# Kernel optimization log

Measured on AMD Instinct MI355X. Metric: run time of the kernel, lower is better.

Reference implementation:

```python
import jax, jax.numpy as jnp
import numpy as np

B_PAIR = 4      # anchor/positive pairs; total batch = 2*B_PAIR
NUM = 4096      # keypoints per cloud
C_FEAT = 640    # descriptor dim
NB_ITER = 5


def _rigid_transform(a, b, weights):
    # a: (B,M,3), b: (B,M,3), weights: (B,M) -> (B,3,4)
    wn = weights[..., None] / (jnp.sum(weights[..., None], axis=1, keepdims=True) + 1e-5)
    centroid_a = jnp.sum(a * wn, axis=1)            # (B,3)
    centroid_b = jnp.sum(b * wn, axis=1)
    a_c = a - centroid_a[:, None, :]
    b_c = b - centroid_b[:, None, :]
    cov = jnp.swapaxes(a_c, -2, -1) @ (b_c * wn)    # (B,3,3)
    u, s, vh = jnp.linalg.svd(cov, full_matrices=False)
    v = jnp.swapaxes(vh, -2, -1)                    # torch.svd returns v, jax returns vh
    rot_pos = v @ jnp.swapaxes(u, -2, -1)
    v_neg = v.at[:, :, 2].multiply(-1.0)
    rot_neg = v_neg @ jnp.swapaxes(u, -2, -1)
    rot = jnp.where(jnp.linalg.det(rot_pos)[:, None, None] > 0, rot_pos, rot_neg)
    trans = -rot @ centroid_a[:, :, None] + centroid_b[:, :, None]
    return jnp.concatenate((rot, trans), axis=2)    # (B,3,4)


def _uot_forward(point_features, point_coords, gamma, epsilon):
    feats = point_features[..., 0]                  # (2B, C, N)
    twoB, _, N = feats.shape
    B = twoB // 2
    feat1 = jnp.transpose(feats[:B], (0, 2, 1))     # (B, N, C)
    feat2 = jnp.transpose(feats[B:], (0, 2, 1))
    coords = point_coords.reshape(twoB, -1, 4)
    coords1 = coords[:B, :, 1:]                     # (B, N, 3)
    coords2 = coords[B:, :, 1:]

    eps = jnp.exp(epsilon) + 0.03                   # scalar (1,)
    gam = jnp.exp(gamma)

    f1 = feat1 / jnp.sqrt(jnp.sum(feat1**2, -1, keepdims=True) + 1e-8)
    f2 = feat2 / jnp.sqrt(jnp.sum(feat2**2, -1, keepdims=True) + 1e-8)
    Cmat = 1.0 - jnp.einsum('bnc,bmc->bnm', f1, f2)  # (B,N,N) cosine cost
    K = jnp.exp(-Cmat / eps)

    power = gam / (gam + eps)
    inv_n = jnp.asarray(1.0 / N, K.dtype)
    a = jnp.full((B, N, 1), inv_n, K.dtype)
    prob1 = jnp.full((B, N, 1), inv_n, K.dtype)
    prob2 = jnp.full((B, N, 1), inv_n, K.dtype)
    b = prob2
    for _ in range(NB_ITER):                        # unrolled unbalanced Sinkhorn
        KTa = jnp.matmul(jnp.swapaxes(K, 1, 2), a)  # (B,N,1)
        b = jnp.power(prob2 / (KTa + 1e-8), power)
        Kb = jnp.matmul(K, b)
        a = jnp.power(prob1 / (Kb + 1e-8), power)
    T = a * K * jnp.swapaxes(b, 1, 2)               # (B,N,N) transport plan

    row_sum = jnp.sum(T, axis=-1, keepdims=True)    # (B,N,1)
    sinkhorn_matches = jnp.matmul(T, coords2) / (row_sum + 1e-8)  # (B,N,3)
    transform = _rigid_transform(coords1, sinkhorn_matches, row_sum[..., 0])
    return T, sinkhorn_matches, transform


def setup_inputs() -> dict:
    key = jax.random.key(0)
    k1, k2 = jax.random.split(key)
    point_features = jax.random.normal(k1, (2 * B_PAIR, C_FEAT, NUM, 1), dtype=jnp.float32)
    point_coords = jax.random.normal(k2, (2 * B_PAIR * NUM, 4), dtype=jnp.float32) * 10.0
    gamma = jnp.zeros((1,), jnp.float32)
    epsilon = jnp.zeros((1,), jnp.float32)
    return {"point_features": point_features, "point_coords": point_coords,
            "gamma": gamma, "epsilon": epsilon}


def reference(point_features, point_coords, gamma, epsilon):
    return _uot_forward(point_features, point_coords, gamma, epsilon)
```

## Files before the change

kernel.cpp:

```cpp
#include <hip/hip_runtime.h>
#include <hip/hip_bf16.h>
#include <math.h>

#define NB 4
#define N 4096
#define CF 640

typedef _Float16 f16;
typedef _Float16 f16x8 __attribute__((ext_vector_type(8)));
typedef _Float16 f16x4 __attribute__((ext_vector_type(4)));
typedef float    f32x4 __attribute__((ext_vector_type(4)));
typedef unsigned int u32;
typedef unsigned short u16;

#define OFF_FNT    0ll
#define OFF_RNORM  (OFF_FNT   + 8ll*N*CF*2)
#define OFF_AVEC   (OFF_RNORM + 8ll*N*4)
#define OFF_BVEC   (OFF_AVEC  + (long long)NB*N*4)
#define OFF_KTAP   (OFF_BVEC  + (long long)NB*N*4)
#define OFF_KH     (OFF_KTAP  + (long long)NB*16*N*4)
#define WS_REQ_H   (OFF_KH    + (long long)NB*N*N*2)

__device__ inline void async_copy16(void* lds, const void* g) {
    __builtin_amdgcn_global_load_lds(
        (const __attribute__((address_space(1))) u32*)g,
        (__attribute__((address_space(3))) u32*)lds,
        16, 0, 0);
}

__global__ __launch_bounds__(256) void rnorm_kernel(const float* __restrict__ pf,
                                                    float* __restrict__ rnorm) {
    int idx = blockIdx.x * 256 + threadIdx.x;
    int n = idx & (N - 1);
    int b = idx >> 12;
    const float* src = pf + (size_t)b * CF * N + n;
    float s = 0.f;
    for (int c = 0; c < CF; ++c) { float v = src[(size_t)c * N]; s = fmaf(v, v, s); }
    rnorm[idx] = 1.0f / sqrtf(s + 1e-8f);
}

__global__ __launch_bounds__(256) void transpose_kernel(const float* __restrict__ pf,
                                                        const float* __restrict__ rnorm,
                                                        f16* __restrict__ fnT) {
    __shared__ float tile[64][65];
    int b  = blockIdx.z;
    int c0 = blockIdx.x * 64;
    int n1 = blockIdx.y * 64;
    int t  = threadIdx.x;

    int c_l = t >> 4;
    int n_l4 = (t & 15) * 4;
    #pragma unroll
    for (int i = 0; i < 4; ++i) {
        int c = c_l + i * 16;
        float4 v = *(const float4*)(pf + (size_t)(b * CF + c0 + c) * N + n1 + n_l4);
        tile[c][n_l4 + 0] = v.x; tile[c][n_l4 + 1] = v.y;
        tile[c][n_l4 + 2] = v.z; tile[c][n_l4 + 3] = v.w;
    }
    __syncthreads();

    int n_l = t >> 2;
    int c_g = (t & 3) * 16;
    float rn = rnorm[b * N + n1 + n_l];
    f16 tmp[16] __attribute__((aligned(16)));
    #pragma unroll
    for (int i = 0; i < 16; ++i)
        tmp[i] = (f16)(tile[c_g + i][n_l] * rn);
    f16* dst = fnT + (size_t)(b * N + n1 + n_l) * CF + c0 + c_g;
    ((uint4*)dst)[0] = ((const uint4*)tmp)[0];
    ((uint4*)dst)[1] = ((const uint4*)tmp)[1];
}

__global__ __launch_bounds__(256) void init_a_kernel(float* __restrict__ avec) {
    int i = blockIdx.x * 256 + threadIdx.x;
    if (i < NB * N) avec[i] = 1.0f / N;
}

__global__ __launch_bounds__(256) void gemm_h_kernel(const f16* __restrict__ fnT,
                                                     const float* __restrict__ e_in,
                                                     float* __restrict__ Kout,
                                                     f16* __restrict__ Kh,
                                                     int write_h) {
    int b  = blockIdx.z;
    int m0 = blockIdx.x * 128;
    int n0 = blockIdx.y * 128;
    const f16* A = fnT + (size_t)b       * N * CF;
    const f16* B = fnT + (size_t)(b + 4) * N * CF;

    __shared__ f16 As[128 * 32];
    __shared__ f16 Bs[128 * 32];

    int tid = threadIdx.x;
    int w = tid >> 6;
    int l = tid & 63;
    int wr = w >> 1, wc = w & 1;

    f32x4 acc[4][4];
    #pragma unroll
    for (int i = 0; i < 4; ++i)
        #pragma unroll
        for (int j = 0; j < 4; ++j)
            acc[i][j] = (f32x4){0.f, 0.f, 0.f, 0.f};

    int srow = l >> 2;
    int scp  = l & 3;

    for (int c0 = 0; c0 < CF; c0 += 32) {
        #pragma unroll
        for (int q = 0; q < 2; ++q) {
            int ch = w * 2 + q;
            int row = ch * 16 + srow;
            int cc = scp ^ ((row >> 1) & 3);
            async_copy16(&As[ch * 512], A + (size_t)(n0 + row) * CF + c0 + cc * 8);
            async_copy16(&Bs[ch * 512], B + (size_t)(m0 + row) * CF + c0 + cc * 8);
        }
        __syncthreads();

        f16x8 af[4], bfr[4];
        int g = l >> 4, low = l & 15;
        #pragma unroll
        for (int t = 0; t < 4; ++t) {
            int rowA = wr * 64 + t * 16 + low;
            af[t] = *(const f16x8*)(As + rowA * 32 + (g ^ ((rowA >> 1) & 3)) * 8);
            int rowB = wc * 64 + t * 16 + low;
            bfr[t] = *(const f16x8*)(Bs + rowB * 32 + (g ^ ((rowB >> 1) & 3)) * 8);
        }
        #pragma unroll
        for (int i = 0; i < 4; ++i)
            #pragma unroll
            for (int j = 0; j < 4; ++j)
                acc[i][j] = __builtin_amdgcn_mfma_f32_16x16x32_f16(af[i], bfr[j], acc[i][j], 0, 0, 0);
        __syncthreads();
    }

    float eps = expf(e_in[0]) + 0.03f;
    float inv_eps = 1.0f / eps;
    float* out = Kout + (size_t)b * N * N;
    f16* oh = Kh + (size_t)b * N * N;
    int g = l >> 4, col = l & 15;
    #pragma unroll
    for (int i = 0; i < 4; ++i) {
        int nb = n0 + wr * 64 + i * 16 + g * 4;
        #pragma unroll
        for (int j = 0; j < 4; ++j) {
            int m = m0 + wc * 64 + j * 16 + col;
            #pragma unroll
            for (int r = 0; r < 4; ++r) {
                float v = expf((acc[i][j][r] - 1.0f) * inv_eps);
                out[(size_t)(nb + r) * N + m] = v;
                if (write_h) oh[(size_t)(nb + r) * N + m] = (f16)v;
            }
        }
    }
}

template<bool H>
__global__ __launch_bounds__(256) void colsum_k(const void* __restrict__ Kp,
                                                const float* __restrict__ avec,
                                                float* __restrict__ ktap) {
    int b = blockIdx.z;
    int chunk = blockIdx.y;
    __shared__ float sh_a[256];
    int n0 = chunk * 256;
    sh_a[threadIdx.x] = avec[b * N + n0 + threadIdx.x];
    __syncthreads();
    if constexpr (H) {
        int m8 = blockIdx.x * 2048 + threadIdx.x * 8;
        const f16* Kb = (const f16*)Kp + (size_t)b * N * N;
        float s[8] = {};
        for (int k = 0; k < 256; ++k) {
            f16x8 v = *(const f16x8*)(Kb + (size_t)(n0 + k) * N + m8);
            float a = sh_a[k];
            #pragma unroll
            for (int q = 0; q < 8; ++q) s[q] = fmaf((float)v[q], a, s[q]);
        }
        float* o = ktap + ((size_t)b * 16 + chunk) * N + m8;
        *(float4*)o       = make_float4(s[0], s[1], s[2], s[3]);
        *((float4*)o + 1) = make_float4(s[4], s[5], s[6], s[7]);
    } else {
        int m4 = blockIdx.x * 1024 + threadIdx.x * 4;
        const float* Kf = (const float*)Kp + (size_t)b * N * N;
        float s0 = 0.f, s1 = 0.f, s2 = 0.f, s3 = 0.f;
        for (int k = 0; k < 256; ++k) {
            float4 v = *(const float4*)(Kf + (size_t)(n0 + k) * N + m4);
            float a = sh_a[k];
            s0 = fmaf(v.x, a, s0); s1 = fmaf(v.y, a, s1);
            s2 = fmaf(v.z, a, s2); s3 = fmaf(v.w, a, s3);
        }
        *(float4*)(ktap + ((size_t)b * 16 + chunk) * N + m4) = make_float4(s0, s1, s2, s3);
    }
}

__global__ __launch_bounds__(256) void bvec_kernel(const float* __restrict__ ktap,
                                                   const float* __restrict__ g_in,
                                                   const float* __restrict__ e_in,
                                                   float* __restrict__ bvec) {
    int i = blockIdx.x * 256 + threadIdx.x;
    int b = i >> 12, m = i & (N - 1);
    const float* p = ktap + (size_t)b * 16 * N + m;
    float s = 0.f;
    #pragma unroll
    for (int k = 0; k < 16; ++k) s += p[(size_t)k * N];
    float eps = expf(e_in[0]) + 0.03f;
    float gam = expf(g_in[0]);
    float power = gam / (gam + eps);
    bvec[i] = powf((1.0f / N) / (s + 1e-8f), power);
}

template<bool H>
__global__ __launch_bounds__(256) void rowsum_k(const void* __restrict__ Kp,
                                                const float* __restrict__ bvec,
                                                const float* __restrict__ g_in,
                                                const float* __restrict__ e_in,
                                                float* __restrict__ avec) {
    int b = blockIdx.y, n = blockIdx.x;
    const float* bv = bvec + b * N;
    float s = 0.f;
    if constexpr (H) {
        const f16* row = (const f16*)Kp + ((size_t)b * N + n) * N;
        for (int m = threadIdx.x * 8; m < N; m += 2048) {
            f16x8 v = *(const f16x8*)(row + m);
            float4 b0 = *(const float4*)(bv + m);
            float4 b1 = *(const float4*)(bv + m + 4);
            s = fmaf((float)v[0], b0.x, s); s = fmaf((float)v[1], b0.y, s);
            s = fmaf((float)v[2], b0.z, s); s = fmaf((float)v[3], b0.w, s);
            s = fmaf((float)v[4], b1.x, s); s = fmaf((float)v[5], b1.y, s);
            s = fmaf((float)v[6], b1.z, s); s = fmaf((float)v[7], b1.w, s);
        }
    } else {
        const float* row = (const float*)Kp + ((size_t)b * N + n) * N;
        for (int m = threadIdx.x * 4; m < N; m += 1024) {
            float4 v = *(const float4*)(row + m);
            float4 b4 = *(const float4*)(bv + m);
            s = fmaf(v.x, b4.x, s); s = fmaf(v.y, b4.y, s);
            s = fmaf(v.z, b4.z, s); s = fmaf(v.w, b4.w, s);
        }
    }
    __shared__ float red[256];
    red[threadIdx.x] = s; __syncthreads();
    for (int off = 128; off; off >>= 1) {
        if (threadIdx.x < off) red[threadIdx.x] += red[threadIdx.x + off];
        __syncthreads();
    }
    if (threadIdx.x == 0) {
        float eps = expf(e_in[0]) + 0.03f;
        float gam = expf(g_in[0]);
        float power = gam / (gam + eps);
        avec[b * N + n] = powf((1.0f / N) / (red[0] + 1e-8f), power);
    }
}

__global__ __launch_bounds__(256) void final_kernel(float* __restrict__ T,
                                                    const float* __restrict__ avec,
                                                    const float* __restrict__ bvec,
                                                    const float* __restrict__ pc,
                                                    float* __restrict__ rowsum,
                                                    float* __restrict__ matches) {
    int b = blockIdx.y, n = blockIdx.x;
    float* row = T + ((size_t)b * N + n) * N;
    const float* bv = bvec + b * N;
    float an = avec[b * N + n];
    const float4* c2 = (const float4*)pc + (size_t)(4 + b) * N;
    float rs = 0.f, s0 = 0.f, s1 = 0.f, s2 = 0.f;
    for (int m = threadIdx.x * 4; m < N; m += 1024) {
        float4 kv = *(const float4*)(row + m);
        float4 b4 = *(const float4*)(bv + m);
        float4 t;
        t.x = an * kv.x * b4.x; t.y = an * kv.y * b4.y;
        t.z = an * kv.z * b4.z; t.w = an * kv.w * b4.w;
        *(float4*)(row + m) = t;
        rs += t.x + t.y + t.z + t.w;
        float4 c0 = c2[m], c1 = c2[m + 1], cc2 = c2[m + 2], c3 = c2[m + 3];
        s0 = fmaf(t.x, c0.y, s0); s1 = fmaf(t.x, c0.z, s1); s2 = fmaf(t.x, c0.w, s2);
        s0 = fmaf(t.y, c1.y, s0); s1 = fmaf(t.y, c1.z, s1); s2 = fmaf(t.y, c1.w, s2);
        s0 = fmaf(t.z, cc2.y, s0); s1 = fmaf(t.z, cc2.z, s1); s2 = fmaf(t.z, cc2.w, s2);
        s0 = fmaf(t.w, c3.y, s0); s1 = fmaf(t.w, c3.z, s1); s2 = fmaf(t.w, c3.w, s2);
    }
    __shared__ float4 red[256];
    red[threadIdx.x] = make_float4(rs, s0, s1, s2); __syncthreads();
    for (int off = 128; off; off >>= 1) {
        if (threadIdx.x < off) {
            float4 o = red[threadIdx.x + off];
            red[threadIdx.x].x += o.x; red[threadIdx.x].y += o.y;
            red[threadIdx.x].z += o.z; red[threadIdx.x].w += o.w;
        }
        __syncthreads();
    }
    if (threadIdx.x == 0) {
        float4 tot = red[0];
        rowsum[b * N + n] = tot.x;
        float inv = 1.0f / (tot.x + 1e-8f);
        float* mo = matches + ((size_t)b * N + n) * 3;
        mo[0] = tot.y * inv; mo[1] = tot.z * inv; mo[2] = tot.w * inv;
    }
}

__global__ __launch_bounds__(256) void transform_kernel(const float* __restrict__ rowsum,
                                                        const float* __restrict__ matches,
                                                        const float* __restrict__ pc,
                                                        float* __restrict__ out) {
    int b = blockIdx.x;
    float vals[16];
    #pragma unroll
    for (int q = 0; q < 16; ++q) vals[q] = 0.f;
    for (int n = threadIdx.x; n < N; n += 256) {
        float w = rowsum[b * N + n];
        float4 c1 = ((const float4*)pc)[(size_t)b * N + n];
        float ax = c1.y, ay = c1.z, az = c1.w;
        const float* mm = matches + ((size_t)b * N + n) * 3;
        float bx = mm[0], by = mm[1], bz = mm[2];
        vals[0] += w;
        vals[1] = fmaf(w, ax, vals[1]); vals[2] = fmaf(w, ay, vals[2]); vals[3] = fmaf(w, az, vals[3]);
        vals[4] = fmaf(w, bx, vals[4]); vals[5] = fmaf(w, by, vals[5]); vals[6] = fmaf(w, bz, vals[6]);
        vals[7]  = fmaf(w * ax, bx, vals[7]);  vals[8]  = fmaf(w * ax, by, vals[8]);  vals[9]  = fmaf(w * ax, bz, vals[9]);
        vals[10] = fmaf(w * ay, bx, vals[10]); vals[11] = fmaf(w * ay, by, vals[11]); vals[12] = fmaf(w * ay, bz, vals[12]);
        vals[13] = fmaf(w * az, bx, vals[13]); vals[14] = fmaf(w * az, by, vals[14]); vals[15] = fmaf(w * az, bz, vals[15]);
    }
    __shared__ float red[256];
    __shared__ float tot[16];
    for (int q = 0; q < 16; ++q) {
        red[threadIdx.x] = vals[q]; __syncthreads();
        for (int off = 128; off; off >>= 1) {
            if (threadIdx.x < off) red[threadIdx.x] += red[threadIdx.x + off];
            __syncthreads();
        }
        if (threadIdx.x == 0) tot[q] = red[0];
        __syncthreads();
    }
    if (threadIdx.x != 0) return;

    double S = tot[0];
    double denom = S + 1e-5;
    double Ca[3], Cb[3], M[3][3], cov[3][3];
    for (int i = 0; i < 3; ++i) { Ca[i] = tot[1 + i] / denom; Cb[i] = tot[4 + i] / denom; }
    for (int i = 0; i < 3; ++i)
        for (int j = 0; j < 3; ++j)
            M[i][j] = tot[7 + i * 3 + j] / denom;
    double s0 = S / denom;
    for (int i = 0; i < 3; ++i)
        for (int j = 0; j < 3; ++j)
            cov[i][j] = M[i][j] - Ca[i] * Cb[j] * (2.0 - s0);

    double Sm[3][3], V[3][3] = {{1,0,0},{0,1,0},{0,0,1}};
    for (int i = 0; i < 3; ++i)
        for (int j = 0; j < 3; ++j) {
            double acc = 0;
            for (int k = 0; k < 3; ++k) acc += cov[k][i] * cov[k][j];
            Sm[i][j] = acc;
        }
    for (int sweep = 0; sweep < 20; ++sweep) {
        static const int pq[3][2] = {{0,1},{0,2},{1,2}};
        for (int r = 0; r < 3; ++r) {
            int p = pq[r][0], q = pq[r][1];
            double apq = Sm[p][q];
            if (fabs(apq) < 1e-30) continue;
            double tau = (Sm[q][q] - Sm[p][p]) / (2.0 * apq);
            double t = (tau >= 0) ? 1.0 / (tau + sqrt(1.0 + tau * tau))
                                  : 1.0 / (tau - sqrt(1.0 + tau * tau));
            double c = 1.0 / sqrt(1.0 + t * t), s = t * c;
            for (int i = 0; i < 3; ++i) {
                double sip = Sm[i][p], siq = Sm[i][q];
                Sm[i][p] = c * sip - s * siq; Sm[i][q] = s * sip + c * siq;
            }
            for (int j = 0; j < 3; ++j) {
                double spj = Sm[p][j], sqj = Sm[q][j];
                Sm[p][j] = c * spj - s * sqj; Sm[q][j] = s * spj + c * sqj;
            }
            for (int i = 0; i < 3; ++i) {
                double vip = V[i][p], viq = V[i][q];
                V[i][p] = c * vip - s * viq; V[i][q] = s * vip + c * viq;
            }
        }
    }
    double lam[3] = {Sm[0][0], Sm[1][1], Sm[2][2]};
    for (int i = 0; i < 2; ++i)
        for (int j = i + 1; j < 3; ++j)
            if (lam[j] > lam[i]) {
                double tl = lam[i]; lam[i] = lam[j]; lam[j] = tl;
                for (int k = 0; k < 3; ++k) { double tv = V[k][i]; V[k][i] = V[k][j]; V[k][j] = tv; }
            }
    double U[3][3];
    double sig0 = sqrt(fmax(lam[0], 0.0));
    for (int j = 0; j < 3; ++j) {
        double sig = sqrt(fmax(lam[j], 0.0));
        if (sig > 1e-12 * (sig0 + 1e-300)) {
            double nrm = 0;
            for (int i = 0; i < 3; ++i) {
                double u = cov[i][0] * V[0][j] + cov[i][1] * V[1][j] + cov[i][2] * V[2][j];
                U[i][j] = u; nrm += u * u;
            }
            nrm = 1.0 / sqrt(nrm + 1e-300);
            for (int i = 0; i < 3; ++i) U[i][j] *= nrm;
        } else {
            U[0][j] = U[1][0] * U[2][1] - U[2][0] * U[1][1];
            U[1][j] = U[2][0] * U[0][1] - U[0][0] * U[2][1];
            U[2][j] = U[0][0] * U[1][1] - U[1][0] * U[0][1];
        }
    }
    double R[3][3];
    for (int i = 0; i < 3; ++i)
        for (int j = 0; j < 3; ++j)
            R[i][j] = V[i][0] * U[j][0] + V[i][1] * U[j][1] + V[i][2] * U[j][2];
    double det = R[0][0] * (R[1][1] * R[2][2] - R[1][2] * R[2][1])
               - R[0][1] * (R[1][0] * R[2][2] - R[1][2] * R[2][0])
               + R[0][2] * (R[1][0] * R[2][1] - R[1][1] * R[2][0]);
    if (!(det > 0)) {
        for (int k = 0; k < 3; ++k) V[k][2] = -V[k][2];
        for (int i = 0; i < 3; ++i)
            for (int j = 0; j < 3; ++j)
                R[i][j] = V[i][0] * U[j][0] + V[i][1] * U[j][1] + V[i][2] * U[j][2];
    }
    double tr[3];
    for (int i = 0; i < 3; ++i)
        tr[i] = -(R[i][0] * Ca[0] + R[i][1] * Ca[1] + R[i][2] * Ca[2]) + Cb[i];
    float* o = out + b * 12;
    for (int i = 0; i < 3; ++i) {
        o[i * 4 + 0] = (float)R[i][0];
        o[i * 4 + 1] = (float)R[i][1];
        o[i * 4 + 2] = (float)R[i][2];
        o[i * 4 + 3] = (float)tr[i];
    }
}

extern "C" void kernel_launch(void* const* d_in, const int* in_sizes, int n_in,
                              void* d_out, int out_size, void* d_ws, size_t ws_size,
                              hipStream_t stream) {
    const float* pf   = (const float*)d_in[0];
    const float* pc   = (const float*)d_in[1];
    const float* g_in = (const float*)d_in[2];
    const float* e_in = (const float*)d_in[3];

    char* wsb = (char*)d_ws;
    f16*   fnT    = (f16*)(wsb + OFF_FNT);
    float* rnorm  = (float*)(wsb + OFF_RNORM);
    float* avec   = (float*)(wsb + OFF_AVEC);
    float* bvec   = (float*)(wsb + OFF_BVEC);
    float* ktap   = (float*)(wsb + OFF_KTAP);
    f16*   Kh     = (f16*)(wsb + OFF_KH);

    float* T_out   = (float*)d_out;
    float* matches = T_out + (size_t)NB * N * N;
    float* trans   = matches + (size_t)NB * N * 3;
    float* rowsum  = rnorm;

    int use_h = (ws_size >= (size_t)WS_REQ_H) ? 1 : 0;

    rnorm_kernel<<<dim3(8 * N / 256), 256, 0, stream>>>(pf, rnorm);
    transpose_kernel<<<dim3(CF / 64, N / 64, 8), 256, 0, stream>>>(pf, rnorm, fnT);
    init_a_kernel<<<dim3(NB * N / 256), 256, 0, stream>>>(avec);

    gemm_h_kernel<<<dim3(N / 128, N / 128, NB), 256, 0, stream>>>(fnT, e_in, T_out, Kh, use_h);

    for (int it = 0; it < 5; ++it) {
        if (use_h) colsum_k<true><<<dim3(N / 2048, 16, NB), 256, 0, stream>>>(Kh, avec, ktap);
        else       colsum_k<false><<<dim3(N / 1024, 16, NB), 256, 0, stream>>>(T_out, avec, ktap);
        bvec_kernel<<<dim3(NB * N / 256), 256, 0, stream>>>(ktap, g_in, e_in, bvec);
        if (use_h) rowsum_k<true><<<dim3(N, NB), 256, 0, stream>>>(Kh, bvec, g_in, e_in, avec);
        else       rowsum_k<false><<<dim3(N, NB), 256, 0, stream>>>(T_out, bvec, g_in, e_in, avec);
    }

    final_kernel<<<dim3(N, NB), 256, 0, stream>>>(T_out, avec, bvec, pc, rowsum, matches);

    transform_kernel<<<dim3(NB), 256, 0, stream>>>(rowsum, matches, pc, trans);
}
```

Before: 1.016 ms.

## Fuse Sinkhorn iterations into slab kernels and fold first column sum into GEMM

The GEMM epilogue now computes per-tile column sums of K (scaled by the initial uniform a), so the first K^T a pass over K is folded into the GEMM. Each later iteration is one slab kernel: it computes row sums K·b for 64 rows, derives a locally, then accumulates those rows' contribution to K^T a while the slab is likely still in cache. This replaces two full passes over K per iteration with one. The final kernel recomputes the last a from the row it already loads, and f16 K stores are staged through LDS for coalesced writes. The trade-off is a 64-way partial-sum buffer and more register and LDS pressure in the GEMM.

```diff
diff --git a/kernel.cpp b/kernel.cpp
--- a/kernel.cpp
+++ b/kernel.cpp
@@ -1,5 +1,4 @@
 #include <hip/hip_runtime.h>
-#include <hip/hip_bf16.h>
 #include <math.h>
 
 #define NB 4
@@ -11,15 +10,14 @@
 typedef _Float16 f16x4 __attribute__((ext_vector_type(4)));
 typedef float    f32x4 __attribute__((ext_vector_type(4)));
 typedef unsigned int u32;
-typedef unsigned short u16;
-
-#define OFF_FNT    0ll
-#define OFF_RNORM  (OFF_FNT   + 8ll*N*CF*2)
-#define OFF_AVEC   (OFF_RNORM + 8ll*N*4)
-#define OFF_BVEC   (OFF_AVEC  + (long long)NB*N*4)
-#define OFF_KTAP   (OFF_BVEC  + (long long)NB*N*4)
-#define OFF_KH     (OFF_KTAP  + (long long)NB*16*N*4)
-#define WS_REQ_H   (OFF_KH    + (long long)NB*N*N*2)
+
+#define OFF_FNT   0ll
+#define OFF_RNORM (OFF_FNT + 8ll*N*CF*2)
+#define OFF_BVEC  (OFF_RNORM + 8ll*N*4)
+#define OFF_SCR   (OFF_BVEC + (long long)NB*N*4)
+#define OFF_KTAP  (OFF_SCR + (long long)NB*N*N*2)
+#define REQ_H     (OFF_KTAP + (long long)NB*64*N*4)
+#define REQ_F     (OFF_SCR + (long long)NB*64*N*4)
 
 __device__ inline void async_copy16(void* lds, const void* g) {
     __builtin_amdgcn_global_load_lds(
@@ -71,24 +69,22 @@
     ((uint4*)dst)[1] = ((const uint4*)tmp)[1];
 }
 
-__global__ __launch_bounds__(256) void init_a_kernel(float* __restrict__ avec) {
-    int i = blockIdx.x * 256 + threadIdx.x;
-    if (i < NB * N) avec[i] = 1.0f / N;
-}
-
-__global__ __launch_bounds__(256) void gemm_h_kernel(const f16* __restrict__ fnT,
-                                                     const float* __restrict__ e_in,
-                                                     float* __restrict__ Kout,
-                                                     f16* __restrict__ Kh,
-                                                     int write_h) {
+template<bool H>
+__global__ __launch_bounds__(256) void gemm_k(const f16* __restrict__ fnT,
+                                              const float* __restrict__ e_in,
+                                              float* __restrict__ Kf,
+                                              f16* __restrict__ Kh,
+                                              float* __restrict__ ktap) {
     int b  = blockIdx.z;
-    int m0 = blockIdx.x * 128;
-    int n0 = blockIdx.y * 128;
+    int m0 = blockIdx.y * 128;
+    int n0 = blockIdx.x * 128;
     const f16* A = fnT + (size_t)b       * N * CF;
     const f16* B = fnT + (size_t)(b + 4) * N * CF;
 
     __shared__ f16 As[128 * 32];
     __shared__ f16 Bs[128 * 32];
+    __shared__ float cs[2][128];
+    __shared__ f16 Ct[H ? 128 * 136 : 1];
 
     int tid = threadIdx.x;
     int w = tid >> 6;
@@ -135,72 +131,59 @@
 
     float eps = expf(e_in[0]) + 0.03f;
     float inv_eps = 1.0f / eps;
-    float* out = Kout + (size_t)b * N * N;
-    f16* oh = Kh + (size_t)b * N * N;
-    int g = l >> 4, col = l & 15;
+    int g4 = l >> 4, low = l & 15;
+    float colp[4] = {0.f, 0.f, 0.f, 0.f};
+    float* out = Kf + (size_t)b * N * N;
+
     #pragma unroll
     for (int i = 0; i < 4; ++i) {
-        int nb = n0 + wr * 64 + i * 16 + g * 4;
+        int rl = wr * 64 + i * 16 + g4 * 4;
         #pragma unroll
         for (int j = 0; j < 4; ++j) {
-            int m = m0 + wc * 64 + j * 16 + col;
+            int cl = wc * 64 + j * 16 + low;
             #pragma unroll
             for (int r = 0; r < 4; ++r) {
                 float v = expf((acc[i][j][r] - 1.0f) * inv_eps);
-                out[(size_t)(nb + r) * N + m] = v;
-                if (write_h) oh[(size_t)(nb + r) * N + m] = (f16)v;
-            }
-        }
-    }
-}
-
-template<bool H>
-__global__ __launch_bounds__(256) void colsum_k(const void* __restrict__ Kp,
-                                                const float* __restrict__ avec,
-                                                float* __restrict__ ktap) {
-    int b = blockIdx.z;
-    int chunk = blockIdx.y;
-    __shared__ float sh_a[256];
-    int n0 = chunk * 256;
-    sh_a[threadIdx.x] = avec[b * N + n0 + threadIdx.x];
+                out[(size_t)(n0 + rl + r) * N + m0 + cl] = v;
+                if constexpr (H) Ct[(rl + r) * 136 + cl] = (f16)v;
+                colp[j] += v;
+            }
+        }
+    }
+
+    #pragma unroll
+    for (int j = 0; j < 4; ++j) {
+        float c = colp[j];
+        c += __shfl_down(c, 32);
+        c += __shfl_down(c, 16);
+        if (l < 16) cs[wr][wc * 64 + j * 16 + l] = c;
+    }
     __syncthreads();
+    if (tid < 128)
+        ktap[((size_t)b * 64 + blockIdx.x) * N + m0 + tid] =
+            (cs[0][tid] + cs[1][tid]) * (1.0f / N);
+
     if constexpr (H) {
-        int m8 = blockIdx.x * 2048 + threadIdx.x * 8;
-        const f16* Kb = (const f16*)Kp + (size_t)b * N * N;
-        float s[8] = {};
-        for (int k = 0; k < 256; ++k) {
-            f16x8 v = *(const f16x8*)(Kb + (size_t)(n0 + k) * N + m8);
-            float a = sh_a[k];
-            #pragma unroll
-            for (int q = 0; q < 8; ++q) s[q] = fmaf((float)v[q], a, s[q]);
-        }
-        float* o = ktap + ((size_t)b * 16 + chunk) * N + m8;
-        *(float4*)o       = make_float4(s[0], s[1], s[2], s[3]);
-        *((float4*)o + 1) = make_float4(s[4], s[5], s[6], s[7]);
-    } else {
-        int m4 = blockIdx.x * 1024 + threadIdx.x * 4;
-        const float* Kf = (const float*)Kp + (size_t)b * N * N;
-        float s0 = 0.f, s1 = 0.f, s2 = 0.f, s3 = 0.f;
-        for (int k = 0; k < 256; ++k) {
-            float4 v = *(const float4*)(Kf + (size_t)(n0 + k) * N + m4);
-            float a = sh_a[k];
-            s0 = fmaf(v.x, a, s0); s1 = fmaf(v.y, a, s1);
-            s2 = fmaf(v.z, a, s2); s3 = fmaf(v.w, a, s3);
-        }
-        *(float4*)(ktap + ((size_t)b * 16 + chunk) * N + m4) = make_float4(s0, s1, s2, s3);
-    }
-}
-
-__global__ __launch_bounds__(256) void bvec_kernel(const float* __restrict__ ktap,
+        f16* oh = Kh + (size_t)b * N * N;
+        int row0 = tid >> 4, c8 = (tid & 15) * 8;
+        #pragma unroll
+        for (int rr = 0; rr < 8; ++rr) {
+            int row = rr * 16 + row0;
+            f16x8 v = *(const f16x8*)(Ct + row * 136 + c8);
+            *(f16x8*)(oh + (size_t)(n0 + row) * N + m0 + c8) = v;
+        }
+    }
+}
+
+__global__ __launch_bounds__(256) void bvec_kernel(const float* __restrict__ ktap, int npart,
                                                    const float* __restrict__ g_in,
                                                    const float* __restrict__ e_in,
                                                    float* __restrict__ bvec) {
     int i = blockIdx.x * 256 + threadIdx.x;
     int b = i >> 12, m = i & (N - 1);
-    const float* p = ktap + (size_t)b * 16 * N + m;
+    const float* p = ktap + (size_t)b * 64 * N + m;
     float s = 0.f;
-    #pragma unroll
-    for (int k = 0; k < 16; ++k) s += p[(size_t)k * N];
+    for (int k = 0; k < npart; ++k) s += p[(size_t)k * N];
     float eps = expf(e_in[0]) + 0.03f;
     float gam = expf(g_in[0]);
     float power = gam / (gam + eps);
@@ -208,86 +191,167 @@
 }
 
 template<bool H>
-__global__ __launch_bounds__(256) void rowsum_k(const void* __restrict__ Kp,
-                                                const float* __restrict__ bvec,
-                                                const float* __restrict__ g_in,
-                                                const float* __restrict__ e_in,
-                                                float* __restrict__ avec) {
+__global__ __launch_bounds__(256) void fused_iter(const void* __restrict__ Kp,
+                                                  const float* __restrict__ bv_in,
+                                                  const float* __restrict__ g_in,
+                                                  const float* __restrict__ e_in,
+                                                  float* __restrict__ ktap) {
+    int b = blockIdx.y, slab = blockIdx.x;
+    int n0s = slab * 64;
+    int w = threadIdx.x >> 6, l = threadIdx.x & 63;
+    __shared__ float ash[64];
+    float eps = expf(e_in[0]) + 0.03f;
+    float gam = expf(g_in[0]);
+    float power = gam / (gam + eps);
+    const float* bv = bv_in + b * N;
+
+    float acc[16];
+    #pragma unroll
+    for (int q = 0; q < 16; ++q) acc[q] = 0.f;
+
+    if constexpr (H) {
+        const f16* Kb = (const f16*)Kp + ((size_t)b * N + n0s) * N;
+        for (int it = 0; it < 8; ++it) {
+            int m = it * 512 + l * 8;
+            float bq[8];
+            *(float4*)&bq[0] = *(const float4*)(bv + m);
+            *(float4*)&bq[4] = *(const float4*)(bv + m + 4);
+            #pragma unroll
+            for (int rr = 0; rr < 16; ++rr) {
+                f16x8 v = *(const f16x8*)(Kb + (size_t)(rr * 4 + w) * N + m);
+                #pragma unroll
+                for (int q = 0; q < 8; ++q) acc[rr] = fmaf((float)v[q], bq[q], acc[rr]);
+            }
+        }
+    } else {
+        const float* Kb = (const float*)Kp + ((size_t)b * N + n0s) * N;
+        for (int it = 0; it < 16; ++it) {
+            int m = it * 256 + l * 4;
+            float4 bq = *(const float4*)(bv + m);
+            #pragma unroll
+            for (int rr = 0; rr < 16; ++rr) {
+                float4 v = *(const float4*)(Kb + (size_t)(rr * 4 + w) * N + m);
+                acc[rr] = fmaf(v.x, bq.x, acc[rr]);
+                acc[rr] = fmaf(v.y, bq.y, acc[rr]);
+                acc[rr] = fmaf(v.z, bq.z, acc[rr]);
+                acc[rr] = fmaf(v.w, bq.w, acc[rr]);
+            }
+        }
+    }
+    #pragma unroll
+    for (int rr = 0; rr < 16; ++rr) {
+        float s = acc[rr];
+        s += __shfl_down(s, 32);
+        s += __shfl_down(s, 16);
+        s += __shfl_down(s, 8);
+        s += __shfl_down(s, 4);
+        s += __shfl_down(s, 2);
+        s += __shfl_down(s, 1);
+        if (l == 0) ash[rr * 4 + w] = powf((1.0f / N) / (s + 1e-8f), power);
+    }
+    __syncthreads();
+
+    float cacc[16];
+    #pragma unroll
+    for (int q = 0; q < 16; ++q) cacc[q] = 0.f;
+    int t4 = threadIdx.x * 4;
+    if constexpr (H) {
+        const f16* Kb = (const f16*)Kp + ((size_t)b * N + n0s) * N;
+        for (int r = 0; r < 64; ++r) {
+            float a = ash[r];
+            #pragma unroll
+            for (int q = 0; q < 4; ++q) {
+                f16x4 v = *(const f16x4*)(Kb + (size_t)r * N + q * 1024 + t4);
+                #pragma unroll
+                for (int j = 0; j < 4; ++j)
+                    cacc[q * 4 + j] = fmaf((float)v[j], a, cacc[q * 4 + j]);
+            }
+        }
+    } else {
+        const float* Kb = (const float*)Kp + ((size_t)b * N + n0s) * N;
+        for (int r = 0; r < 64; ++r) {
+            float a = ash[r];
+            #pragma unroll
+            for (int q = 0; q < 4; ++q) {
+                float4 v = *(const float4*)(Kb + (size_t)r * N + q * 1024 + t4);
+                cacc[q * 4 + 0] = fmaf(v.x, a, cacc[q * 4 + 0]);
+                cacc[q * 4 + 1] = fmaf(v.y, a, cacc[q * 4 + 1]);
+                cacc[q * 4 + 2] = fmaf(v.z, a, cacc[q * 4 + 2]);
+                cacc[q * 4 + 3] = fmaf(v.w, a, cacc[q * 4 + 3]);
+            }
+        }
+    }
+    float* o = ktap + ((size_t)b * 64 + slab) * N;
+    #pragma unroll
+    for (int q = 0; q < 4; ++q)
+        *(float4*)(o + q * 1024 + t4) =
+            make_float4(cacc[q * 4], cacc[q * 4 + 1], cacc[q * 4 + 2], cacc[q * 4 + 3]);
+}
+
+__global__ __launch_bounds__(256) void final_k(float* __restrict__ Tout,
+                                               const float* __restrict__ bv_in,
+                                               const float* __restrict__ g_in,
+                                               const float* __restrict__ e_in,
+                                               const float* __restrict__ pc,
+                                               float* __restrict__ rowsum,
+                                               float* __restrict__ matches) {
     int b = blockIdx.y, n = blockIdx.x;
-    const float* bv = bvec + b * N;
+    int t = threadIdx.x;
+    int t4 = t * 4;
+    const float* bv = bv_in + b * N;
+    float kv[16], bl[16];
+    float* Trow = Tout + ((size_t)b * N + n) * N;
+    #pragma unroll
+    for (int q = 0; q < 4; ++q) {
+        *(float4*)&bl[q * 4] = *(const float4*)(bv + q * 1024 + t4);
+        *(float4*)&kv[q * 4] = *(const float4*)(Trow + q * 1024 + t4);
+    }
     float s = 0.f;
-    if constexpr (H) {
-        const f16* row = (const f16*)Kp + ((size_t)b * N + n) * N;
-        for (int m = threadIdx.x * 8; m < N; m += 2048) {
-            f16x8 v = *(const f16x8*)(row + m);
-            float4 b0 = *(const float4*)(bv + m);
-            float4 b1 = *(const float4*)(bv + m + 4);
-            s = fmaf((float)v[0], b0.x, s); s = fmaf((float)v[1], b0.y, s);
-            s = fmaf((float)v[2], b0.z, s); s = fmaf((float)v[3], b0.w, s);
-            s = fmaf((float)v[4], b1.x, s); s = fmaf((float)v[5], b1.y, s);
-            s = fmaf((float)v[6], b1.z, s); s = fmaf((float)v[7], b1.w, s);
-        }
-    } else {
-        const float* row = (const float*)Kp + ((size_t)b * N + n) * N;
-        for (int m = threadIdx.x * 4; m < N; m += 1024) {
-            float4 v = *(const float4*)(row + m);
-            float4 b4 = *(const float4*)(bv + m);
-            s = fmaf(v.x, b4.x, s); s = fmaf(v.y, b4.y, s);
-            s = fmaf(v.z, b4.z, s); s = fmaf(v.w, b4.w, s);
-        }
-    }
+    #pragma unroll
+    for (int q = 0; q < 16; ++q) s = fmaf(kv[q], bl[q], s);
     __shared__ float red[256];
-    red[threadIdx.x] = s; __syncthreads();
+    red[t] = s; __syncthreads();
     for (int off = 128; off; off >>= 1) {
-        if (threadIdx.x < off) red[threadIdx.x] += red[threadIdx.x + off];
+        if (t < off) red[t] += red[t + off];
         __syncthreads();
     }
-    if (threadIdx.x == 0) {
+    __shared__ float a_sh;
+    if (t == 0) {
         float eps = expf(e_in[0]) + 0.03f;
         float gam = expf(g_in[0]);
         float power = gam / (gam + eps);
-        avec[b * N + n] = powf((1.0f / N) / (red[0] + 1e-8f), power);
-    }
-}
-
-__global__ __launch_bounds__(256) void final_kernel(float* __restrict__ T,
-                                                    const float* __restrict__ avec,
-                                                    const float* __restrict__ bvec,
-                                                    const float* __restrict__ pc,
-                                                    float* __restrict__ rowsum,
-                                                    float* __restrict__ matches) {
-    int b = blockIdx.y, n = blockIdx.x;
-    float* row = T + ((size_t)b * N + n) * N;
-    const float* bv = bvec + b * N;
-    float an = avec[b * N + n];
+        a_sh = powf((1.0f / N) / (red[0] + 1e-8f), power);
+    }
+    __syncthreads();
+    float an = a_sh;
     const float4* c2 = (const float4*)pc + (size_t)(4 + b) * N;
     float rs = 0.f, s0 = 0.f, s1 = 0.f, s2 = 0.f;
-    for (int m = threadIdx.x * 4; m < N; m += 1024) {
-        float4 kv = *(const float4*)(row + m);
-        float4 b4 = *(const float4*)(bv + m);
-        float4 t;
-        t.x = an * kv.x * b4.x; t.y = an * kv.y * b4.y;
-        t.z = an * kv.z * b4.z; t.w = an * kv.w * b4.w;
-        *(float4*)(row + m) = t;
-        rs += t.x + t.y + t.z + t.w;
-        float4 c0 = c2[m], c1 = c2[m + 1], cc2 = c2[m + 2], c3 = c2[m + 3];
-        s0 = fmaf(t.x, c0.y, s0); s1 = fmaf(t.x, c0.z, s1); s2 = fmaf(t.x, c0.w, s2);
-        s0 = fmaf(t.y, c1.y, s0); s1 = fmaf(t.y, c1.z, s1); s2 = fmaf(t.y, c1.w, s2);
-        s0 = fmaf(t.z, cc2.y, s0); s1 = fmaf(t.z, cc2.z, s1); s2 = fmaf(t.z, cc2.w, s2);
-        s0 = fmaf(t.w, c3.y, s0); s1 = fmaf(t.w, c3.z, s1); s2 = fmaf(t.w, c3.w, s2);
-    }
-    __shared__ float4 red[256];
-    red[threadIdx.x] = make_float4(rs, s0, s1, s2); __syncthreads();
+    #pragma unroll
+    for (int q = 0; q < 4; ++q) {
+        float tv0 = an * kv[q * 4 + 0] * bl[q * 4 + 0];
+        float tv1 = an * kv[q * 4 + 1] * bl[q * 4 + 1];
+        float tv2 = an * kv[q * 4 + 2] * bl[q * 4 + 2];
+        float tv3 = an * kv[q * 4 + 3] * bl[q * 4 + 3];
+        *(float4*)(Trow + q * 1024 + t4) = make_float4(tv0, tv1, tv2, tv3);
+        rs += tv0 + tv1 + tv2 + tv3;
+        float4 c0 = c2[q * 1024 + t4],     c1 = c2[q * 1024 + t4 + 1],
+               cc = c2[q * 1024 + t4 + 2], c3 = c2[q * 1024 + t4 + 3];
+        s0 = fmaf(tv0, c0.y, s0); s1 = fmaf(tv0, c0.z, s1); s2 = fmaf(tv0, c0.w, s2);
+        s0 = fmaf(tv1, c1.y, s0); s1 = fmaf(tv1, c1.z, s1); s2 = fmaf(tv1, c1.w, s2);
+        s0 = fmaf(tv2, cc.y, s0); s1 = fmaf(tv2, cc.z, s1); s2 = fmaf(tv2, cc.w, s2);
+        s0 = fmaf(tv3, c3.y, s0); s1 = fmaf(tv3, c3.z, s1); s2 = fmaf(tv3, c3.w, s2);
+    }
+    __shared__ float4 red4[256];
+    red4[t] = make_float4(rs, s0, s1, s2); __syncthreads();
     for (int off = 128; off; off >>= 1) {
-        if (threadIdx.x < off) {
-            float4 o = red[threadIdx.x + off];
-            red[threadIdx.x].x += o.x; red[threadIdx.x].y += o.y;
-            red[threadIdx.x].z += o.z; red[threadIdx.x].w += o.w;
+        if (t < off) {
+            float4 o = red4[t + off];
+            red4[t].x += o.x; red4[t].y += o.y; red4[t].z += o.z; red4[t].w += o.w;
         }
         __syncthreads();
     }
-    if (threadIdx.x == 0) {
-        float4 tot = red[0];
+    if (t == 0) {
+        float4 tot = red4[0];
         rowsum[b * N + n] = tot.x;
         float inv = 1.0f / (tot.x + 1e-8f);
         float* mo = matches + ((size_t)b * N + n) * 3;
@@ -431,35 +495,38 @@
     const float* e_in = (const float*)d_in[3];
 
     char* wsb = (char*)d_ws;
-    f16*   fnT    = (f16*)(wsb + OFF_FNT);
-    float* rnorm  = (float*)(wsb + OFF_RNORM);
-    float* avec   = (float*)(wsb + OFF_AVEC);
-    float* bvec   = (float*)(wsb + OFF_BVEC);
-    float* ktap   = (float*)(wsb + OFF_KTAP);
-    f16*   Kh     = (f16*)(wsb + OFF_KH);
+    f16*   fnT   = (f16*)(wsb + OFF_FNT);
+    float* rnorm = (float*)(wsb + OFF_RNORM);
+    float* bvec  = (float*)(wsb + OFF_BVEC);
 
     float* T_out   = (float*)d_out;
     float* matches = T_out + (size_t)NB * N * N;
     float* trans   = matches + (size_t)NB * N * 3;
     float* rowsum  = rnorm;
 
-    int use_h = (ws_size >= (size_t)WS_REQ_H) ? 1 : 0;
-
     rnorm_kernel<<<dim3(8 * N / 256), 256, 0, stream>>>(pf, rnorm);
     transpose_kernel<<<dim3(CF / 64, N / 64, 8), 256, 0, stream>>>(pf, rnorm, fnT);
-    init_a_kernel<<<dim3(NB * N / 256), 256, 0, stream>>>(avec);
-
-    gemm_h_kernel<<<dim3(N / 128, N / 128, NB), 256, 0, stream>>>(fnT, e_in, T_out, Kh, use_h);
-
-    for (int it = 0; it < 5; ++it) {
-        if (use_h) colsum_k<true><<<dim3(N / 2048, 16, NB), 256, 0, stream>>>(Kh, avec, ktap);
-        else       colsum_k<false><<<dim3(N / 1024, 16, NB), 256, 0, stream>>>(T_out, avec, ktap);
-        bvec_kernel<<<dim3(NB * N / 256), 256, 0, stream>>>(ktap, g_in, e_in, bvec);
-        if (use_h) rowsum_k<true><<<dim3(N, NB), 256, 0, stream>>>(Kh, bvec, g_in, e_in, avec);
-        else       rowsum_k<false><<<dim3(N, NB), 256, 0, stream>>>(T_out, bvec, g_in, e_in, avec);
-    }
-
-    final_kernel<<<dim3(N, NB), 256, 0, stream>>>(T_out, avec, bvec, pc, rowsum, matches);
+
+    if (ws_size >= (size_t)REQ_H) {
+        f16*   Kh   = (f16*)(wsb + OFF_SCR);
+        float* ktap = (float*)(wsb + OFF_KTAP);
+        gemm_k<true><<<dim3(N / 128, N / 128, NB), 256, 0, stream>>>(fnT, e_in, T_out, Kh, ktap);
+        bvec_kernel<<<dim3(NB * N / 256), 256, 0, stream>>>(ktap, 32, g_in, e_in, bvec);
+        for (int it = 0; it < 4; ++it) {
+            fused_iter<true><<<dim3(64, NB), 256, 0, stream>>>(Kh, bvec, g_in, e_in, ktap);
+            bvec_kernel<<<dim3(NB * N / 256), 256, 0, stream>>>(ktap, 64, g_in, e_in, bvec);
+        }
+        final_k<<<dim3(N, NB), 256, 0, stream>>>(T_out, bvec, g_in, e_in, pc, rowsum, matches);
+    } else {
+        float* ktap = (float*)(wsb + OFF_SCR);
+        gemm_k<false><<<dim3(N / 128, N / 128, NB), 256, 0, stream>>>(fnT, e_in, T_out, (f16*)nullptr, ktap);
+        bvec_kernel<<<dim3(NB * N / 256), 256, 0, stream>>>(ktap, 32, g_in, e_in, bvec);
+        for (int it = 0; it < 4; ++it) {
+            fused_iter<false><<<dim3(64, NB), 256, 0, stream>>>(T_out, bvec, g_in, e_in, ktap);
+            bvec_kernel<<<dim3(NB * N / 256), 256, 0, stream>>>(ktap, 64, g_in, e_in, bvec);
+        }
+        final_k<<<dim3(N, NB), 256, 0, stream>>>(T_out, bvec, g_in, e_in, pc, rowsum, matches);
+    }
 
     transform_kernel<<<dim3(NB), 256, 0, stream>>>(rowsum, matches, pc, trans);
 }
```

After: 996.8 us. No clear change (-1.9%).
